# Performance work log

Hardware: AMD Instinct MI355X
Metric: run time of the kernel (lower is better)

Reference implementation:

```python
import jax, jax.numpy as jnp
import numpy as np

B = 16384        # batch
NDIS = 20        # discrete features
NCONT = 10       # continuous features
VOCAB = 100000   # per-feature vocab size
EMB = 32         # embedding_size
E = 8            # expert_num
T = 2            # task_num
H1, H2 = 512, 256  # expert hidden units
DOUT = 128       # expert_out_dim
TH = 64          # task hidden units
DIN = NDIS * EMB + NCONT  # 650 expert input dim
GIN = NDIS + NCONT        # 30 gate input dim


def setup_inputs() -> dict:
    key = jax.random.key(0)
    ks = jax.random.split(key, 20)
    s = 0.02
    return {
        "X_dis": jax.random.randint(ks[0], (B, NDIS), 0, VOCAB, dtype=jnp.int32),
        "X_cont": jax.random.normal(ks[1], (B, NCONT), dtype=jnp.float32),
        # embedding tables (stacked across the NDIS features)
        "lin_emb": jax.random.normal(ks[2], (NDIS, VOCAB, 1), dtype=jnp.float32) * s,
        "deep_emb": jax.random.normal(ks[3], (NDIS, VOCAB, EMB), dtype=jnp.float32) * s,
        # expert MLPs stacked across experts: 650 -> 512 -> 256 -> 128
        "expert_W1": jax.random.normal(ks[4], (E, DIN, H1), dtype=jnp.float32) * s,
        "expert_b1": jnp.zeros((E, H1), dtype=jnp.float32),
        "expert_W2": jax.random.normal(ks[5], (E, H1, H2), dtype=jnp.float32) * s,
        "expert_b2": jnp.zeros((E, H2), dtype=jnp.float32),
        "expert_W3": jax.random.normal(ks[6], (E, H2, DOUT), dtype=jnp.float32) * s,
        "expert_b3": jnp.zeros((E, DOUT), dtype=jnp.float32),
        # per-task gate: Linear(30 -> E)
        "gate_W": jax.random.normal(ks[7], (T, GIN, E), dtype=jnp.float32) * s,
        "gate_b": jnp.zeros((T, E), dtype=jnp.float32),
        # per-task tower: 128 -> 64 -> 1
        "task_W1": jax.random.normal(ks[8], (T, DOUT, TH), dtype=jnp.float32) * s,
        "task_b1": jnp.zeros((T, TH), dtype=jnp.float32),
        "task_W2": jax.random.normal(ks[9], (T, TH, 1), dtype=jnp.float32) * s,
        "task_b2": jnp.zeros((T, 1), dtype=jnp.float32),
    }


def reference(X_dis, X_cont, lin_emb, deep_emb,
              expert_W1, expert_b1, expert_W2, expert_b2, expert_W3, expert_b3,
              gate_W, gate_b, task_W1, task_b1, task_W2, task_b2):
    fidx = jnp.arange(NDIS)[None, :]                      # [1, NDIS]
    # batched embedding gathers across all discrete features
    lin = lin_emb[fidx, X_dis][..., 0]                    # [B, NDIS]
    deep = deep_emb[fidx, X_dis].reshape(X_dis.shape[0], -1)  # [B, NDIS*EMB]
    expert_in = jnp.concatenate([deep, X_cont], axis=1)   # [B, 650]
    gate_in = jnp.concatenate([lin, X_cont], axis=1)      # [B, 30]

    # grouped expert MLPs
    h = jax.nn.relu(jnp.einsum('bi,eih->beh', expert_in, expert_W1) + expert_b1)
    h = jax.nn.relu(jnp.einsum('beh,eho->beo', h, expert_W2) + expert_b2)
    expert_out = jnp.einsum('beh,ehd->bed', h, expert_W3) + expert_b3  # [B, E, DOUT]

    # per-task softmax gates and weighted combine
    gates = jax.nn.softmax(jnp.einsum('bi,tie->bte', gate_in, gate_W) + gate_b, axis=-1)
    task_in = jnp.einsum('bte,bed->btd', gates, expert_out)            # [B, T, DOUT]

    # task towers
    t = jax.nn.relu(jnp.einsum('btd,tdh->bth', task_in, task_W1) + task_b1)
    out = (jnp.einsum('bth,tho->bto', t, task_W2) + task_b2)[..., 0]   # [B, T]
    return out
```

## Files before the change

### kernel.cpp

```cpp
#include <hip/hip_runtime.h>


typedef unsigned short u16;
typedef unsigned int u32;
typedef __attribute__((ext_vector_type(8))) __bf16 bf16x8;
typedef __attribute__((ext_vector_type(4))) float f32x4;

#define DEVINL __device__ __forceinline__

DEVINL u16 f2bf(float f) {
  union { float f; u32 u; } x; x.f = f;
  u32 u = x.u;
  return (u16)((u + 0x7fffu + ((u >> 16) & 1u)) >> 16);
}
DEVINL float bf2f(u16 h) {
  union { u32 u; float f; } x; x.u = ((u32)h) << 16;
  return x.f;
}
DEVINL void gload16(const u16* g, u16* l) {
  __builtin_amdgcn_global_load_lds((const __attribute__((address_space(1))) void*)g,
                                   (__attribute__((address_space(3))) void*)l,
                                   16, 0, 0);
}

__global__ __launch_bounds__(256)
void transpose_w_kernel(const float* __restrict__ W, u16* __restrict__ WT,
                        int K, int N, int Kpad)
{
  __shared__ float tbuf[16][65];
  const int e = blockIdx.z;
  const float* We = W + (size_t)e * K * N;
  u16* Wt = WT + (size_t)e * N * Kpad;
  const int k0 = blockIdx.x * 16, n0 = blockIdx.y * 64;
#pragma unroll
  for (int p = 0; p < 4; ++p) {
    const int idx = threadIdx.x + p * 256;
    const int nl = idx & 63, kl = idx >> 6;
    const int gk = k0 + kl;
    tbuf[kl][nl] = (gk < K) ? We[(size_t)gk * N + n0 + nl] : 0.f;
  }
  __syncthreads();
#pragma unroll
  for (int p = 0; p < 4; ++p) {
    const int idx = threadIdx.x + p * 256;
    const int kl = idx & 15, nl = idx >> 4;
    Wt[(size_t)(n0 + nl) * Kpad + k0 + kl] = f2bf(tbuf[kl][nl]);
  }
}

__global__ __launch_bounds__(256)
void gather_kernel(const int* __restrict__ Xd, const float* __restrict__ Xc,
                   const float* __restrict__ lin_emb, const float* __restrict__ deep_emb,
                   const float* __restrict__ gW, const float* __restrict__ gb,
                   u16* __restrict__ ein, float* __restrict__ gates,
                   int rowBase, int Bc)
{
  __shared__ float gi[4][32];
  const int wid = threadIdx.x >> 6, lane = threadIdx.x & 63;
  const int rl = blockIdx.x * 4 + wid;
  const int r = rowBase + rl;
  const int* xd = Xd + (size_t)r * 20;
  u16* er = ein + (size_t)rl * 704;
#pragma unroll
  for (int i = 0; i < 10; ++i) {
    const int j = i * 64 + lane;
    const int f = j >> 5, k = j & 31;
    const int idx = xd[f];
    er[j] = f2bf(deep_emb[((size_t)f * 100000 + idx) * 32 + k]);
  }
  if (lane < 10) er[640 + lane] = f2bf(Xc[(size_t)r * 10 + lane]);
  if (lane < 54) er[650 + lane] = 0;
  if (lane < 20) gi[wid][lane] = lin_emb[(size_t)lane * 100000 + xd[lane]];
  if (lane < 10) gi[wid][20 + lane] = Xc[(size_t)r * 10 + lane];
  asm volatile("s_waitcnt lgkmcnt(0)" ::: "memory");
  float logit = 0.f;
  const int t = lane >> 3, ee = lane & 7;
  if (lane < 16) {
    float a = gb[t * 8 + ee];
#pragma unroll
    for (int i = 0; i < 30; ++i) a += gi[wid][i] * gW[(t * 30 + i) * 8 + ee];
    logit = a;
  }
  float mx = logit;
#pragma unroll
  for (int d = 1; d < 8; d <<= 1) mx = fmaxf(mx, __shfl_xor(mx, d));
  float p = expf(logit - mx);
  float sm = p;
#pragma unroll
  for (int d = 1; d < 8; d <<= 1) sm += __shfl_xor(sm, d);
  if (lane < 16) gates[(size_t)rl * 16 + lane] = p / sm;
}

template<bool RELU, typename CT>
__global__ __launch_bounds__(256, 2)
void gemm_kernel(const u16* __restrict__ A, size_t sAe,
                 const u16* __restrict__ Bw, size_t sBe,
                 CT* __restrict__ C, size_t sCe, int ldc,
                 const float* __restrict__ bias, int N, int K)
{
  __shared__ u16 As[2][8192];
  __shared__ u16 Bs[2][8192];
  const int e = blockIdx.z;
  const u16* Ae = A + (size_t)e * sAe;
  const u16* Be = Bw + (size_t)e * sBe;
  const int row0 = blockIdx.y * 128;
  const int col0 = blockIdx.x * 128;
  const int tid = threadIdx.x;
  const int lane = tid & 63;
  const int wid = tid >> 6;
  const int wr = wid >> 1, wc = wid & 1;

  int rw_[4], gch_[4], ldsOff_[4];
#pragma unroll
  for (int i = 0; i < 4; ++i) {
    const int o = (wid * 4 + i) * 1024 + lane * 16;
    rw_[i] = o >> 7;
    const int ch = (o >> 4) & 7;
    gch_[i] = ch ^ (rw_[i] & 7);
    ldsOff_[i] = (wid * 4 + i) * 512;
  }
  const int KT = K >> 6;

  auto stage = [&](int buf, int kt) {
    const int kb = kt << 6;
#pragma unroll
    for (int i = 0; i < 4; ++i) {
      gload16(Ae + ((size_t)(row0 + rw_[i]) * K + kb + (gch_[i] << 3)),
              &As[buf][ldsOff_[i]]);
      gload16(Be + ((size_t)(col0 + rw_[i]) * K + kb + (gch_[i] << 3)),
              &Bs[buf][ldsOff_[i]]);
    }
  };

  f32x4 acc[4][4];
#pragma unroll
  for (int m = 0; m < 4; ++m)
#pragma unroll
    for (int n = 0; n < 4; ++n) acc[m][n] = {0.f, 0.f, 0.f, 0.f};

  stage(0, 0);
  __syncthreads();

  for (int kt = 0; kt < KT; ++kt) {
    const int cur = kt & 1;
    if (kt + 1 < KT) stage(cur ^ 1, kt + 1);
#pragma unroll
    for (int half = 0; half < 2; ++half) {
      const int kp = half * 4 + (lane >> 4);
      bf16x8 af[4], bfr[4];
#pragma unroll
      for (int m = 0; m < 4; ++m) {
        const int rw = wr * 64 + m * 16 + (lane & 15);
        af[m] = *(const bf16x8*)&As[cur][rw * 64 + ((kp ^ (rw & 7)) << 3)];
      }
#pragma unroll
      for (int n = 0; n < 4; ++n) {
        const int rw = wc * 64 + n * 16 + (lane & 15);
        bfr[n] = *(const bf16x8*)&Bs[cur][rw * 64 + ((kp ^ (rw & 7)) << 3)];
      }
#pragma unroll
      for (int m = 0; m < 4; ++m)
#pragma unroll
        for (int n = 0; n < 4; ++n)
          acc[m][n] = __builtin_amdgcn_mfma_f32_16x16x32_bf16(af[m], bfr[n],
                                                              acc[m][n], 0, 0, 0);
    }
    __syncthreads();
  }

  const int cl = lane & 15;
  const int rl4 = (lane >> 4) * 4;
#pragma unroll
  for (int n = 0; n < 4; ++n) {
    const int col = col0 + wc * 64 + n * 16 + cl;
    const float bv = bias[(size_t)e * N + col];
#pragma unroll
    for (int m = 0; m < 4; ++m) {
      const int grow = row0 + wr * 64 + m * 16 + rl4;
      CT* cp = C + (size_t)e * sCe + (size_t)grow * ldc + col;
#pragma unroll
      for (int j = 0; j < 4; ++j) {
        float v = acc[m][n][j] + bv;
        if (RELU) v = fmaxf(v, 0.f);
        if constexpr (sizeof(CT) == 2) cp[(size_t)j * ldc] = (CT)f2bf(v);
        else                           cp[(size_t)j * ldc] = (CT)v;
      }
    }
  }
}

__global__ __launch_bounds__(256)
void tower_kernel(const float* __restrict__ eo,
                  const float* __restrict__ gates,
                  const float* __restrict__ tW1,
                  const float* __restrict__ tb1,
                  const float* __restrict__ tW2,
                  const float* __restrict__ tb2,
                  float* __restrict__ out,
                  int rowBase, int Bc)
{
  __shared__ u16 w1s[2 * 128 * 64];
  __shared__ float tin[4][2][128];
  for (int i = threadIdx.x; i < 2 * 128 * 64; i += 256) w1s[i] = f2bf(tW1[i]);
  __syncthreads();
  const int wid = threadIdx.x >> 6, lane = threadIdx.x & 63;
  const int stride = gridDim.x * 4;
  for (int it = 0; it < 4; ++it) {
    const int r = blockIdx.x * 4 + wid + it * stride;
    const float* gp = gates + (size_t)r * 16;
    float g[16];
#pragma unroll
    for (int i = 0; i < 16; ++i) g[i] = gp[i];
    float t0a = 0.f, t0b = 0.f, t1a = 0.f, t1b = 0.f;
#pragma unroll
    for (int ee = 0; ee < 8; ++ee) {
      const float* ep = eo + ((size_t)ee * Bc + r) * 128;
      const float a = ep[lane], b = ep[64 + lane];
      t0a += g[ee] * a;      t0b += g[ee] * b;
      t1a += g[8 + ee] * a;  t1b += g[8 + ee] * b;
    }
    tin[wid][0][lane] = t0a; tin[wid][0][64 + lane] = t0b;
    tin[wid][1][lane] = t1a; tin[wid][1][64 + lane] = t1b;
    asm volatile("s_waitcnt lgkmcnt(0)" ::: "memory");
#pragma unroll
    for (int t = 0; t < 2; ++t) {
      float acc = tb1[t * 64 + lane];
#pragma unroll 8
      for (int d = 0; d < 128; ++d)
        acc += tin[wid][t][d] * bf2f(w1s[(t * 128 + d) * 64 + lane]);
      acc = fmaxf(acc, 0.f);
      float s = acc * tW2[t * 64 + lane];
#pragma unroll
      for (int dd = 1; dd < 64; dd <<= 1) s += __shfl_xor(s, dd);
      if (lane == 0) out[(size_t)(rowBase + r) * 2 + t] = s + tb2[t];
    }
    asm volatile("s_waitcnt lgkmcnt(0)" ::: "memory");
  }
}

extern "C" void kernel_launch(void* const* d_in, const int* in_sizes, int n_in,
                              void* d_out, int out_size, void* d_ws, size_t ws_size,
                              hipStream_t stream) {
  const int*   X_dis   = (const int*)  d_in[0];
  const float* X_cont  = (const float*)d_in[1];
  const float* lin_emb = (const float*)d_in[2];
  const float* deep_emb= (const float*)d_in[3];
  const float* eW1     = (const float*)d_in[4];
  const float* eb1     = (const float*)d_in[5];
  const float* eW2     = (const float*)d_in[6];
  const float* eb2     = (const float*)d_in[7];
  const float* eW3     = (const float*)d_in[8];
  const float* eb3     = (const float*)d_in[9];
  const float* gW      = (const float*)d_in[10];
  const float* gb      = (const float*)d_in[11];
  const float* tW1     = (const float*)d_in[12];
  const float* tb1     = (const float*)d_in[13];
  const float* tW2     = (const float*)d_in[14];
  const float* tb2     = (const float*)d_in[15];
  float* out = (float*)d_out;

  char* ws = (char*)d_ws;
  u16* w1t = (u16*)(ws + 0);
  u16* w2t = (u16*)(ws + 5767168);
  u16* w3t = (u16*)(ws + 7864320);
  const size_t base = 8388608;

  const int B = 16384;
  int NC = 1;
  while (NC < 128 && base + (size_t)(B / NC) * 13760ull > ws_size) NC <<= 1;
  const int Bc = B / NC;

  u16*   ein   = (u16*)  (ws + base);
  float* gates = (float*)(ws + base + (size_t)Bc * 1408);
  u16*   h1    = (u16*)  (ws + base + (size_t)Bc * 1472);
  u16*   h2    = (u16*)  (ws + base + (size_t)Bc * 1472 + (size_t)Bc * 8192);
  float* eo    = (float*)h1;

  transpose_w_kernel<<<dim3(44, 8, 8), 256, 0, stream>>>(eW1, w1t, 650, 512, 704);
  transpose_w_kernel<<<dim3(32, 4, 8), 256, 0, stream>>>(eW2, w2t, 512, 256, 512);
  transpose_w_kernel<<<dim3(16, 2, 8), 256, 0, stream>>>(eW3, w3t, 256, 128, 256);

  for (int c = 0; c < NC; ++c) {
    const int rowBase = c * Bc;
    gather_kernel<<<Bc / 4, 256, 0, stream>>>(X_dis, X_cont, lin_emb, deep_emb,
                                              gW, gb, ein, gates, rowBase, Bc);
    gemm_kernel<true,  u16><<<dim3(4, Bc / 128, 8), 256, 0, stream>>>(
        ein, 0,                 w1t, (size_t)512 * 704,
        h1, (size_t)Bc * 512, 512, eb1, 512, 704);
    gemm_kernel<true,  u16><<<dim3(2, Bc / 128, 8), 256, 0, stream>>>(
        h1, (size_t)Bc * 512,   w2t, (size_t)256 * 512,
        h2, (size_t)Bc * 256, 256, eb2, 256, 512);
    gemm_kernel<false, float><<<dim3(1, Bc / 128, 8), 256, 0, stream>>>(
        h2, (size_t)Bc * 256,   w3t, (size_t)128 * 256,
        eo, (size_t)Bc * 128, 128, eb3, 128, 256);
    tower_kernel<<<Bc / 16, 256, 0, stream>>>(eo, gates, tW1, tb1, tW2, tb2,
                                              out, rowBase, Bc);
  }
}
```

Measured before the change: 310.9 us.

## Enlarge GEMM tiles with triple-buffered pipeline, vectorize gather, bf16 expert outputs

The GEMM kernel now runs 512 threads over 256x128 tiles with a three-stage LDS ring buffer, vmcnt-based waits and raised MFMA priority, so global loads overlap compute and the B tile is reused across more rows. The embedding gather reads float4 per lane instead of scalars. The third expert GEMM writes bf16 instead of fp32, and the tower kernel reads the packed bf16 values, halving that intermediate traffic. Costs are larger LDS use (which may cap occupancy) and reduced precision for the expert outputs.

```diff
diff --git a/kernel.cpp b/kernel.cpp
--- a/kernel.cpp
+++ b/kernel.cpp
@@ -5,6 +5,7 @@
 typedef unsigned int u32;
 typedef __attribute__((ext_vector_type(8))) __bf16 bf16x8;
 typedef __attribute__((ext_vector_type(4))) float f32x4;
+typedef __attribute__((ext_vector_type(4))) unsigned short u16x4;
 
 #define DEVINL __device__ __forceinline__
 
@@ -62,11 +63,16 @@
   const int* xd = Xd + (size_t)r * 20;
   u16* er = ein + (size_t)rl * 704;
 #pragma unroll
-  for (int i = 0; i < 10; ++i) {
-    const int j = i * 64 + lane;
-    const int f = j >> 5, k = j & 31;
-    const int idx = xd[f];
-    er[j] = f2bf(deep_emb[((size_t)f * 100000 + idx) * 32 + k]);
+  for (int i = 0; i < 3; ++i) {
+    const int li = i * 64 + lane;
+    if (li < 160) {
+      const int f = li >> 3, sub = li & 7;
+      const int idx = xd[f];
+      const float4 v = *(const float4*)&deep_emb[((size_t)f * 100000 + idx) * 32 + sub * 4];
+      u16x4 o;
+      o.x = f2bf(v.x); o.y = f2bf(v.y); o.z = f2bf(v.z); o.w = f2bf(v.w);
+      *(u16x4*)&er[f * 32 + sub * 4] = o;
+    }
   }
   if (lane < 10) er[640 + lane] = f2bf(Xc[(size_t)r * 10 + lane]);
   if (lane < 54) er[650 + lane] = 0;
@@ -92,43 +98,42 @@
 }
 
 template<bool RELU, typename CT>
-__global__ __launch_bounds__(256, 2)
+__global__ __launch_bounds__(512, 2)
 void gemm_kernel(const u16* __restrict__ A, size_t sAe,
                  const u16* __restrict__ Bw, size_t sBe,
                  CT* __restrict__ C, size_t sCe, int ldc,
                  const float* __restrict__ bias, int N, int K)
 {
-  __shared__ u16 As[2][8192];
-  __shared__ u16 Bs[2][8192];
+  __shared__ u16 As[3][16384];
+  __shared__ u16 Bs[3][8192];
   const int e = blockIdx.z;
   const u16* Ae = A + (size_t)e * sAe;
   const u16* Be = Bw + (size_t)e * sBe;
-  const int row0 = blockIdx.y * 128;
+  const int row0 = blockIdx.y * 256;
   const int col0 = blockIdx.x * 128;
   const int tid = threadIdx.x;
   const int lane = tid & 63;
   const int wid = tid >> 6;
   const int wr = wid >> 1, wc = wid & 1;
-
-  int rw_[4], gch_[4], ldsOff_[4];
-#pragma unroll
-  for (int i = 0; i < 4; ++i) {
-    const int o = (wid * 4 + i) * 1024 + lane * 16;
-    rw_[i] = o >> 7;
-    const int ch = (o >> 4) & 7;
-    gch_[i] = ch ^ (rw_[i] & 7);
-    ldsOff_[i] = (wid * 4 + i) * 512;
-  }
   const int KT = K >> 6;
 
+  const int r8 = tid >> 3;
+  const int ch = tid & 7;
   auto stage = [&](int buf, int kt) {
     const int kb = kt << 6;
 #pragma unroll
     for (int i = 0; i < 4; ++i) {
-      gload16(Ae + ((size_t)(row0 + rw_[i]) * K + kb + (gch_[i] << 3)),
-              &As[buf][ldsOff_[i]]);
-      gload16(Be + ((size_t)(col0 + rw_[i]) * K + kb + (gch_[i] << 3)),
-              &Bs[buf][ldsOff_[i]]);
+      const int rr = i * 64 + r8;
+      const int gc = ch ^ (rr & 7);
+      gload16(Ae + ((size_t)(row0 + rr) * K + kb + (gc << 3)),
+              &As[buf][i * 4096 + tid * 8]);
+    }
+#pragma unroll
+    for (int i = 0; i < 2; ++i) {
+      const int rr = i * 64 + r8;
+      const int gc = ch ^ (rr & 7);
+      gload16(Be + ((size_t)(col0 + rr) * K + kb + (gc << 3)),
+              &Bs[buf][i * 4096 + tid * 8]);
     }
   };
 
@@ -139,11 +144,18 @@
     for (int n = 0; n < 4; ++n) acc[m][n] = {0.f, 0.f, 0.f, 0.f};
 
   stage(0, 0);
-  __syncthreads();
-
-  for (int kt = 0; kt < KT; ++kt) {
-    const int cur = kt & 1;
-    if (kt + 1 < KT) stage(cur ^ 1, kt + 1);
+  if (KT > 1) stage(1, 1);
+
+  int cur = 0, nx2 = 2;
+  for (int t = 0; t < KT; ++t) {
+    if (t + 1 < KT) { asm volatile("s_waitcnt vmcnt(6)" ::: "memory"); }
+    else            { asm volatile("s_waitcnt vmcnt(0)" ::: "memory"); }
+    __builtin_amdgcn_s_barrier();
+    asm volatile("" ::: "memory");
+    __builtin_amdgcn_sched_barrier(0);
+    if (t + 2 < KT) stage(nx2, t + 2);
+    const u16* as = &As[cur][0];
+    const u16* bs = &Bs[cur][0];
 #pragma unroll
     for (int half = 0; half < 2; ++half) {
       const int kp = half * 4 + (lane >> 4);
@@ -151,21 +163,24 @@
 #pragma unroll
       for (int m = 0; m < 4; ++m) {
         const int rw = wr * 64 + m * 16 + (lane & 15);
-        af[m] = *(const bf16x8*)&As[cur][rw * 64 + ((kp ^ (rw & 7)) << 3)];
+        af[m] = *(const bf16x8*)&as[rw * 64 + ((kp ^ (rw & 7)) << 3)];
       }
 #pragma unroll
       for (int n = 0; n < 4; ++n) {
         const int rw = wc * 64 + n * 16 + (lane & 15);
-        bfr[n] = *(const bf16x8*)&Bs[cur][rw * 64 + ((kp ^ (rw & 7)) << 3)];
+        bfr[n] = *(const bf16x8*)&bs[rw * 64 + ((kp ^ (rw & 7)) << 3)];
       }
+      __builtin_amdgcn_s_setprio(1);
 #pragma unroll
       for (int m = 0; m < 4; ++m)
 #pragma unroll
         for (int n = 0; n < 4; ++n)
           acc[m][n] = __builtin_amdgcn_mfma_f32_16x16x32_bf16(af[m], bfr[n],
                                                               acc[m][n], 0, 0, 0);
-    }
-    __syncthreads();
+      __builtin_amdgcn_s_setprio(0);
+    }
+    cur = (cur == 2) ? 0 : cur + 1;
+    nx2 = (nx2 == 2) ? 0 : nx2 + 1;
   }
 
   const int cl = lane & 15;
@@ -190,13 +205,11 @@
 }
 
 __global__ __launch_bounds__(256)
-void tower_kernel(const float* __restrict__ eo,
+void tower_kernel(const u16* __restrict__ eo,
                   const float* __restrict__ gates,
                   const float* __restrict__ tW1,
-                  const float* __restrict__ tb1,
-                  const float* __restrict__ tW2,
-                  const float* __restrict__ tb2,
-                  float* __restrict__ out,
+                  const float* __restrict__ tb1, const float* __restrict__ tW2,
+                  const float* __restrict__ tb2, float* __restrict__ out,
                   int rowBase, int Bc)
 {
   __shared__ u16 w1s[2 * 128 * 64];
@@ -214,13 +227,14 @@
     float t0a = 0.f, t0b = 0.f, t1a = 0.f, t1b = 0.f;
 #pragma unroll
     for (int ee = 0; ee < 8; ++ee) {
-      const float* ep = eo + ((size_t)ee * Bc + r) * 128;
-      const float a = ep[lane], b = ep[64 + lane];
+      const u32 pv = *(const u32*)(eo + ((size_t)ee * Bc + r) * 128 + lane * 2);
+      const float a = bf2f((u16)(pv & 0xffff));
+      const float b = bf2f((u16)(pv >> 16));
       t0a += g[ee] * a;      t0b += g[ee] * b;
       t1a += g[8 + ee] * a;  t1b += g[8 + ee] * b;
     }
-    tin[wid][0][lane] = t0a; tin[wid][0][64 + lane] = t0b;
-    tin[wid][1][lane] = t1a; tin[wid][1][64 + lane] = t1b;
+    tin[wid][0][lane * 2] = t0a; tin[wid][0][lane * 2 + 1] = t0b;
+    tin[wid][1][lane * 2] = t1a; tin[wid][1][lane * 2 + 1] = t1b;
     asm volatile("s_waitcnt lgkmcnt(0)" ::: "memory");
 #pragma unroll
     for (int t = 0; t < 2; ++t) {
@@ -267,14 +281,14 @@
 
   const int B = 16384;
   int NC = 1;
-  while (NC < 128 && base + (size_t)(B / NC) * 13760ull > ws_size) NC <<= 1;
+  while (NC < 64 && base + (size_t)(B / NC) * 13760ull > ws_size) NC <<= 1;
   const int Bc = B / NC;
 
   u16*   ein   = (u16*)  (ws + base);
   float* gates = (float*)(ws + base + (size_t)Bc * 1408);
   u16*   h1    = (u16*)  (ws + base + (size_t)Bc * 1472);
   u16*   h2    = (u16*)  (ws + base + (size_t)Bc * 1472 + (size_t)Bc * 8192);
-  float* eo    = (float*)h1;
+  u16*   eo    = h1;
 
   transpose_w_kernel<<<dim3(44, 8, 8), 256, 0, stream>>>(eW1, w1t, 650, 512, 704);
   transpose_w_kernel<<<dim3(32, 4, 8), 256, 0, stream>>>(eW2, w2t, 512, 256, 512);
@@ -284,13 +298,13 @@
     const int rowBase = c * Bc;
     gather_kernel<<<Bc / 4, 256, 0, stream>>>(X_dis, X_cont, lin_emb, deep_emb,
                                               gW, gb, ein, gates, rowBase, Bc);
-    gemm_kernel<true,  u16><<<dim3(4, Bc / 128, 8), 256, 0, stream>>>(
+    gemm_kernel<true,  u16><<<dim3(4, Bc / 256, 8), 512, 0, stream>>>(
         ein, 0,                 w1t, (size_t)512 * 704,
         h1, (size_t)Bc * 512, 512, eb1, 512, 704);
-    gemm_kernel<true,  u16><<<dim3(2, Bc / 128, 8), 256, 0, stream>>>(
+    gemm_kernel<true,  u16><<<dim3(2, Bc / 256, 8), 512, 0, stream>>>(
         h1, (size_t)Bc * 512,   w2t, (size_t)256 * 512,
         h2, (size_t)Bc * 256, 256, eb2, 256, 512);
-    gemm_kernel<false, float><<<dim3(1, Bc / 128, 8), 256, 0, stream>>>(
+    gemm_kernel<false, u16><<<dim3(1, Bc / 256, 8), 512, 0, stream>>>(
         h2, (size_t)Bc * 256,   w3t, (size_t)128 * 256,
         eo, (size_t)Bc * 128, 128, eb3, 128, 256);
     tower_kernel<<<Bc / 16, 256, 0, stream>>>(eo, gates, tW1, tb1, tW2, tb2,
```

After: 341.9 us. +10.0%, slower.

## Vectorize gather, remap GEMM blocks across experts, store expert output as bf16

Applied to the files above, without the earlier changes.

The gather loads embedding rows with float4 reads and writes packed bf16 instead of scalar loads. The GEMM grid is flattened to 1D and remapped so that consecutive blocks land on different experts, and the MFMA section is wrapped in s_setprio. The third GEMM now writes bf16 instead of fp32, and the tower reads packed bf16 pairs. The chunk-count cap is also lowered. Together these aim to cut memory traffic and improve scheduling, at the cost of slightly lower precision in the expert outputs.

```diff
diff --git a/kernel.cpp b/kernel.cpp
--- a/kernel.cpp
+++ b/kernel.cpp
@@ -5,6 +5,7 @@
 typedef unsigned int u32;
 typedef __attribute__((ext_vector_type(8))) __bf16 bf16x8;
 typedef __attribute__((ext_vector_type(4))) float f32x4;
+typedef __attribute__((ext_vector_type(4))) unsigned short u16x4;
 
 #define DEVINL __device__ __forceinline__
 
@@ -62,11 +63,16 @@
   const int* xd = Xd + (size_t)r * 20;
   u16* er = ein + (size_t)rl * 704;
 #pragma unroll
-  for (int i = 0; i < 10; ++i) {
-    const int j = i * 64 + lane;
-    const int f = j >> 5, k = j & 31;
-    const int idx = xd[f];
-    er[j] = f2bf(deep_emb[((size_t)f * 100000 + idx) * 32 + k]);
+  for (int i = 0; i < 3; ++i) {
+    const int li = i * 64 + lane;
+    if (li < 160) {
+      const int f = li >> 3, sub = li & 7;
+      const int idx = xd[f];
+      const float4 v = *(const float4*)&deep_emb[((size_t)f * 100000 + idx) * 32 + sub * 4];
+      u16x4 o;
+      o.x = f2bf(v.x); o.y = f2bf(v.y); o.z = f2bf(v.z); o.w = f2bf(v.w);
+      *(u16x4*)&er[f * 32 + sub * 4] = o;
+    }
   }
   if (lane < 10) er[640 + lane] = f2bf(Xc[(size_t)r * 10 + lane]);
   if (lane < 54) er[650 + lane] = 0;
@@ -96,15 +102,23 @@
 void gemm_kernel(const u16* __restrict__ A, size_t sAe,
                  const u16* __restrict__ Bw, size_t sBe,
                  CT* __restrict__ C, size_t sCe, int ldc,
-                 const float* __restrict__ bias, int N, int K)
+                 const float* __restrict__ bias, int N, int K,
+                 int nCol, int nRow)
 {
   __shared__ u16 As[2][8192];
   __shared__ u16 Bs[2][8192];
-  const int e = blockIdx.z;
+
+  const int perE = nCol * nRow;
+  const int work = (blockIdx.x & 7) * perE + (blockIdx.x >> 3);
+  const int e  = work / perE;
+  const int rem = work - e * perE;
+  const int mt = rem / nCol;
+  const int ct = rem - mt * nCol;
+
   const u16* Ae = A + (size_t)e * sAe;
   const u16* Be = Bw + (size_t)e * sBe;
-  const int row0 = blockIdx.y * 128;
-  const int col0 = blockIdx.x * 128;
+  const int row0 = mt * 128;
+  const int col0 = ct * 128;
   const int tid = threadIdx.x;
   const int lane = tid & 63;
   const int wid = tid >> 6;
@@ -158,12 +172,14 @@
         const int rw = wc * 64 + n * 16 + (lane & 15);
         bfr[n] = *(const bf16x8*)&Bs[cur][rw * 64 + ((kp ^ (rw & 7)) << 3)];
       }
+      __builtin_amdgcn_s_setprio(1);
 #pragma unroll
       for (int m = 0; m < 4; ++m)
 #pragma unroll
         for (int n = 0; n < 4; ++n)
           acc[m][n] = __builtin_amdgcn_mfma_f32_16x16x32_bf16(af[m], bfr[n],
                                                               acc[m][n], 0, 0, 0);
+      __builtin_amdgcn_s_setprio(0);
     }
     __syncthreads();
   }
@@ -190,13 +206,11 @@
 }
 
 __global__ __launch_bounds__(256)
-void tower_kernel(const float* __restrict__ eo,
+void tower_kernel(const u16* __restrict__ eo,
                   const float* __restrict__ gates,
                   const float* __restrict__ tW1,
-                  const float* __restrict__ tb1,
-                  const float* __restrict__ tW2,
-                  const float* __restrict__ tb2,
-                  float* __restrict__ out,
+                  const float* __restrict__ tb1, const float* __restrict__ tW2,
+                  const float* __restrict__ tb2, float* __restrict__ out,
                   int rowBase, int Bc)
 {
   __shared__ u16 w1s[2 * 128 * 64];
@@ -214,13 +228,14 @@
     float t0a = 0.f, t0b = 0.f, t1a = 0.f, t1b = 0.f;
 #pragma unroll
     for (int ee = 0; ee < 8; ++ee) {
-      const float* ep = eo + ((size_t)ee * Bc + r) * 128;
-      const float a = ep[lane], b = ep[64 + lane];
+      const u32 pv = *(const u32*)(eo + ((size_t)ee * Bc + r) * 128 + lane * 2);
+      const float a = bf2f((u16)(pv & 0xffff));
+      const float b = bf2f((u16)(pv >> 16));
       t0a += g[ee] * a;      t0b += g[ee] * b;
       t1a += g[8 + ee] * a;  t1b += g[8 + ee] * b;
     }
-    tin[wid][0][lane] = t0a; tin[wid][0][64 + lane] = t0b;
-    tin[wid][1][lane] = t1a; tin[wid][1][64 + lane] = t1b;
+    tin[wid][0][lane * 2] = t0a; tin[wid][0][lane * 2 + 1] = t0b;
+    tin[wid][1][lane * 2] = t1a; tin[wid][1][lane * 2 + 1] = t1b;
     asm volatile("s_waitcnt lgkmcnt(0)" ::: "memory");
 #pragma unroll
     for (int t = 0; t < 2; ++t) {
@@ -267,14 +282,14 @@
 
   const int B = 16384;
   int NC = 1;
-  while (NC < 128 && base + (size_t)(B / NC) * 13760ull > ws_size) NC <<= 1;
+  while (NC < 64 && base + (size_t)(B / NC) * 13760ull > ws_size) NC <<= 1;
   const int Bc = B / NC;
 
   u16*   ein   = (u16*)  (ws + base);
   float* gates = (float*)(ws + base + (size_t)Bc * 1408);
   u16*   h1    = (u16*)  (ws + base + (size_t)Bc * 1472);
   u16*   h2    = (u16*)  (ws + base + (size_t)Bc * 1472 + (size_t)Bc * 8192);
-  float* eo    = (float*)h1;
+  u16*   eo    = h1;
 
   transpose_w_kernel<<<dim3(44, 8, 8), 256, 0, stream>>>(eW1, w1t, 650, 512, 704);
   transpose_w_kernel<<<dim3(32, 4, 8), 256, 0, stream>>>(eW2, w2t, 512, 256, 512);
@@ -282,17 +297,18 @@
 
   for (int c = 0; c < NC; ++c) {
     const int rowBase = c * Bc;
+    const int nRow = Bc / 128;
     gather_kernel<<<Bc / 4, 256, 0, stream>>>(X_dis, X_cont, lin_emb, deep_emb,
                                               gW, gb, ein, gates, rowBase, Bc);
-    gemm_kernel<true,  u16><<<dim3(4, Bc / 128, 8), 256, 0, stream>>>(
+    gemm_kernel<true,  u16><<<4 * nRow * 8, 256, 0, stream>>>(
         ein, 0,                 w1t, (size_t)512 * 704,
-        h1, (size_t)Bc * 512, 512, eb1, 512, 704);
-    gemm_kernel<true,  u16><<<dim3(2, Bc / 128, 8), 256, 0, stream>>>(
+        h1, (size_t)Bc * 512, 512, eb1, 512, 704, 4, nRow);
+    gemm_kernel<true,  u16><<<2 * nRow * 8, 256, 0, stream>>>(
         h1, (size_t)Bc * 512,   w2t, (size_t)256 * 512,
-        h2, (size_t)Bc * 256, 256, eb2, 256, 512);
-    gemm_kernel<false, float><<<dim3(1, Bc / 128, 8), 256, 0, stream>>>(
+        h2, (size_t)Bc * 256, 256, eb2, 256, 512, 2, nRow);
+    gemm_kernel<false, u16><<<1 * nRow * 8, 256, 0, stream>>>(
         h2, (size_t)Bc * 256,   w3t, (size_t)128 * 256,
-        eo, (size_t)Bc * 128, 128, eb3, 128, 256);
+        eo, (size_t)Bc * 128, 128, eb3, 128, 256, 1, nRow);
     tower_kernel<<<Bc / 16, 256, 0, stream>>>(eo, gates, tW1, tb1, tW2, tb2,
                                               out, rowBase, Bc);
   }
```

Measured after the change: 267.4 us. 14.0% less time.
